# Kernel optimization log

Hardware: AMD Instinct MI355X
Metric: run time of the kernel (lower is better)

The kernel has to match this reference:

```python
import jax, jax.numpy as jnp
import numpy as np

IN_H = IN_W = 128
OUT_H = OUT_W = 512
CHUNK = 65536  # = 256*256, same chunk size as the torch while-loop
EPS = 1e-6


def _conv3(x, w, b):
    y = jax.lax.conv_general_dilated(x, w, (1, 1), ((1, 1), (1, 1)),
                                     dimension_numbers=('NCHW', 'OIHW', 'NCHW'))
    return y + b[None, :, None, None]


def _centers(n):
    # torch.arange(-1,1,2/n)+1/n  ==  cell centers in (-1,1)
    return (jnp.arange(n, dtype=jnp.float32) + 0.5) * (2.0 / n) - 1.0


def setup_inputs() -> dict:
    key = jax.random.key(0)
    ks = iter(jax.random.split(key, 40))
    rnd = lambda shape, s: jax.random.normal(next(ks), shape, jnp.float32) * s
    inp = {
        'x': jax.random.uniform(next(ks), (1, 3, IN_H, IN_W), jnp.float32),
        'output_size': jnp.array([OUT_H, OUT_W], dtype=jnp.int32),
        # EDSR encoder params
        'head_w': rnd((64, 3, 3, 3), 0.05), 'head_b': rnd((64,), 0.01),
        'rb_w': rnd((16, 2, 64, 64, 3, 3), 0.02), 'rb_b': rnd((16, 2, 64), 0.01),
        'tail_w': rnd((64, 64, 3, 3), 0.02), 'tail_b': rnd((64,), 0.01),
        # MLP 580 -> 256 -> 256 -> 256 -> 256 -> 3
        'mw0': rnd((580, 256), 0.04), 'mb0': rnd((256,), 0.01),
        'mw1': rnd((256, 256), 0.06), 'mb1': rnd((256,), 0.01),
        'mw2': rnd((256, 256), 0.06), 'mb2': rnd((256,), 0.01),
        'mw3': rnd((256, 256), 0.06), 'mb3': rnd((256,), 0.01),
        'mw4': rnd((256, 3), 0.06), 'mb4': rnd((3,), 0.01),
    }
    return inp


def reference(x, output_size, head_w, head_b, rb_w, rb_b, tail_w, tail_b,
              mw0, mb0, mw1, mb1, mw2, mb2, mw3, mb3, mw4, mb4):
    # ---- EDSR encoder (head conv + 16 resblocks + tail conv, residual) ----
    h0 = _conv3(x, head_w, head_b)

    def block(h, wb):
        w0, b0, w1, b1 = wb
        return h + _conv3(jax.nn.relu(_conv3(h, w0, b0)), w1, b1), None

    hb, _ = jax.lax.scan(block, h0, (rb_w[:, 0], rb_b[:, 0], rb_w[:, 1], rb_b[:, 1]))
    feat64 = h0 + _conv3(hb, tail_w, tail_b)  # [1,64,H,W]
    B, C, H, W = feat64.shape

    # im2col 3x3 pad 1 -> channel order (c, kh, kw), matching torch im2col.view
    p = jnp.pad(feat64, ((0, 0), (0, 0), (1, 1), (1, 1)))
    feat = jnp.stack([p[:, :, i:i + H, j:j + W]
                      for i in range(3) for j in range(3)],
                     axis=2).reshape(B, C * 9, H, W)  # [1,576,H,W]

    # normalized cell-center coordinate map of the feature grid: [2,H,W], (h,w)
    fg = jnp.stack(jnp.meshgrid(_centers(H), _centers(W), indexing='ij'))

    ws = (mw0, mw1, mw2, mw3, mw4)
    bs = (mb0, mb1, mb2, mb3, mb4)

    def mlp(t):
        for w, b in zip(ws[:-1], bs[:-1]):
            t = jax.nn.relu(t @ w + b)
        return t @ ws[-1] + bs[-1]

    dh, dw = 1.0 / H, 1.0 / W
    hw = jnp.array([H, W], jnp.float32)
    q_cell = jnp.array([2.0 * H / OUT_H, 2.0 * W / OUT_W], jnp.float32)
    fimg = feat[0]  # [576,H,W]

    def sample(img, gh, gw):
        # torch grid_sampler nearest, align_corners=False, round-half-to-even
        iy = jnp.clip(jnp.round(((gh + 1.0) * H - 1.0) * 0.5), 0, H - 1).astype(jnp.int32)
        ix = jnp.clip(jnp.round(((gw + 1.0) * W - 1.0) * 0.5), 0, W - 1).astype(jnp.int32)
        return img[:, iy, ix].T  # [P, C]

    def query_chunk(s_grid):  # [P,2] = (h,w) normalized coords
        preds, areas = [], []
        for r in (0, 1):
            for c in (0, 1):
                gh = jnp.clip(s_grid[:, 0] + (2.0 * r - 1.0) * dh, -1 + EPS, 1 - EPS)
                gw = jnp.clip(s_grid[:, 1] + (2.0 * c - 1.0) * dw, -1 + EPS, 1 - EPS)
                q_feat = sample(fimg, gh, gw)            # [P,576]
                q_grid = sample(fg, gh, gw)              # [P,2]
                rel = (s_grid - q_grid) * hw             # [P,2]
                inp = jnp.concatenate(
                    [q_feat, rel, jnp.broadcast_to(q_cell, rel.shape)], axis=-1)
                preds.append(mlp(inp))                   # [P,3]
                areas.append(jnp.abs(rel[:, 0] * rel[:, 1]))
        tot = areas[0] + areas[1] + areas[2] + areas[3] + 1e-9
        # LIIF local ensembling with swapped (diagonal) areas
        num = (preds[0] * areas[3][:, None] + preds[1] * areas[2][:, None]
               + preds[2] * areas[1][:, None] + preds[3] * areas[0][:, None])
        return num / tot[:, None]

    grid = jnp.stack(jnp.meshgrid(_centers(OUT_H), _centers(OUT_W), indexing='ij'),
                     axis=-1).reshape(-1, 2)             # [n,2]
    chunks = grid.reshape(-1, CHUNK, 2)                  # [nc,CHUNK,2]
    ys = jax.lax.map(query_chunk, chunks)                # [nc,CHUNK,3]
    y = ys.reshape(OUT_H, OUT_W, 3).transpose(2, 0, 1)[None]  # [1,3,OH,OW]
    return jnp.clip(y, 0.0, 1.0)
```

## Files before the change

kernel.cpp:

```cpp
#include <hip/hip_runtime.h>
#include <hip/hip_fp16.h>

typedef __attribute__((ext_vector_type(8))) _Float16 half8;
typedef __attribute__((ext_vector_type(4))) _Float16 half4;
typedef __attribute__((ext_vector_type(4))) float float4v;

#define NPIX 16384

__device__ inline half8 h8zero() {
    half8 z = {(_Float16)0, (_Float16)0, (_Float16)0, (_Float16)0,
               (_Float16)0, (_Float16)0, (_Float16)0, (_Float16)0};
    return z;
}

__global__ void pack_all(const float* __restrict__ rb_w, const float* __restrict__ tail_w,
                         const float* __restrict__ mw0, const float* __restrict__ mw1,
                         const float* __restrict__ mw2, const float* __restrict__ mw3,
                         const float* __restrict__ mw4, const float* __restrict__ mb0,
                         const float* __restrict__ x, const float* __restrict__ head_w,
                         const float* __restrict__ head_b,
                         _Float16* __restrict__ pwc, _Float16* __restrict__ pw0,
                         _Float16* __restrict__ pwm, float* __restrict__ b0p,
                         _Float16* __restrict__ h0) {
    int idx = blockIdx.x * 256 + threadIdx.x;
    if (idx < 1216512) {
        int ci = idx / 36864;
        int e  = idx % 36864;
        int j = e & 7, ln = (e >> 3) & 63, kcnt = e >> 9;
        int kc = kcnt % 18, ntc = kcnt / 18;
        int k = kc * 32 + (ln >> 4) * 8 + j;
        int nn = ntc * 16 + (ln & 15);
        int ij = k >> 6, c = k & 63;
        const float* src = (ci < 32) ? (rb_w + ci * 36864) : tail_w;
        pwc[idx] = (_Float16)src[(nn * 64 + c) * 9 + ij];
        return;
    }
    idx -= 1216512;
    if (idx < 147456) {
        int j = idx & 7, ln = (idx >> 3) & 63, kcnt = idx >> 9;
        int kc = kcnt % 18, ntc = kcnt / 18;
        int k = kc * 32 + (ln >> 4) * 8 + j;
        int nn = ntc * 16 + (ln & 15);
        int ij = k >> 6, c = k & 63;
        pw0[idx] = (_Float16)mw0[(c * 9 + ij) * 256 + nn];
        return;
    }
    idx -= 147456;
    if (idx < 200704) {
        if (idx < 196608) {
            int l = idx / 65536;
            int e = idx % 65536;
            int j = e & 7, ln = (e >> 3) & 63, kcnt = e >> 9;
            int kc = kcnt & 7, ntc = kcnt >> 3;
            int k = kc * 32 + (ln >> 4) * 8 + j;
            int nn = ntc * 16 + (ln & 15);
            const float* w = (l == 0) ? mw1 : ((l == 1) ? mw2 : mw3);
            pwm[idx] = (_Float16)w[k * 256 + nn];
        } else {
            int e = idx - 196608;
            int j = e & 7, ln = (e >> 3) & 63, kc = e >> 9;
            int k = kc * 32 + (ln >> 4) * 8 + j;
            int nn = ln & 15;
            pwm[idx] = (nn < 3) ? (_Float16)mw4[k * 3 + nn] : (_Float16)0.0f;
        }
        return;
    }
    idx -= 200704;
    if (idx < 256) {
        b0p[idx] = mb0[idx] + 0.5f * (mw0[578 * 256 + idx] + mw0[579 * 256 + idx]);
        return;
    }
    idx -= 256;
    if (idx < NPIX * 64) {
        int o = idx & 63, p = idx >> 6;
        int py = p >> 7, px = p & 127;
        float acc = head_b[o];
        #pragma unroll
        for (int c = 0; c < 3; ++c)
            #pragma unroll
            for (int i = 0; i < 3; ++i)
                #pragma unroll
                for (int jj = 0; jj < 3; ++jj) {
                    int y = py + i - 1, xx = px + jj - 1;
                    if (y >= 0 && y < 128 && xx >= 0 && xx < 128)
                        acc += x[c * 16384 + y * 128 + xx]
                             * head_w[((o * 3 + c) * 3 + i) * 3 + jj];
                }
        h0[idx] = (_Float16)acc;
    }
}

#define LDS_STRIDE 72

template <int DH, int DW, int SW, int SOFF, int RES, int ROFF, int INW>
__device__ __forceinline__ void conv_stage(
    const _Float16* __restrict__ src, _Float16* __restrict__ dst,
    _Float16* __restrict__ INb, const _Float16* __restrict__ resg,
    const _Float16* __restrict__ pw, const float* __restrict__ bias,
    int q, int r, int nb, int gy0, int gx0, _Float16* __restrict__ gout)
{
    half8 B[18];
    #pragma unroll
    for (int kc = 0; kc < 18; ++kc)
        B[kc] = *(const half8*)(pw + ((((nb >> 4) * 18 + kc) * 64 + (q << 4) + r) << 3));
    float bv = bias[nb + r];
    constexpr int NPXc = DH * DW;
    constexpr int NT = (NPXc + 15) >> 4;
    #pragma unroll 1
    for (int tl = 0; tl < NT; ++tl) {
        int pa = tl * 16 + r;
        int ca = pa < NPXc ? pa : NPXc - 1;
        int my = ca / DW, mx = ca % DW;
        float4v acc = {0.f, 0.f, 0.f, 0.f};
        #pragma unroll
        for (int kc = 0; kc < 18; ++kc) {
            int ij = kc >> 1;
            int di = ij / 3 - 1;
            int dj = ij % 3 - 1;
            int cb = ((kc & 1) << 5) + (q << 3);
            int sp = (my + 1 + di + SOFF) * SW + (mx + 1 + dj + SOFF);
            half8 a = *(const half8*)(src + sp * LDS_STRIDE + cb);
            acc = __builtin_amdgcn_mfma_f32_16x16x32_f16(a, B[kc], acc, 0, 0, 0);
        }
        #pragma unroll
        for (int reg = 0; reg < 4; ++reg) {
            int pc = tl * 16 + (q << 2) + reg;
            if (pc >= NPXc) continue;
            int dy = pc / DW, dx = pc % DW;
            int gy = gy0 + dy, gx = gx0 + dx;
            bool valid = (gy >= 0 && gy < 128 && gx >= 0 && gx < 128);
            if (RES == 0) {
                float v = fmaxf(acc[reg] + bv, 0.f);
                dst[pc * LDS_STRIDE + nb + r] = valid ? (_Float16)v : (_Float16)0.0f;
            } else if (RES == 1) {
                int sl = ((dy + ROFF) * INW + dx + ROFF) * LDS_STRIDE + nb + r;
                float v = acc[reg] + bv + (float)INb[sl];
                INb[sl] = valid ? (_Float16)v : (_Float16)0.0f;
            } else if (RES == 2) {
                int sl = ((dy + ROFF) * INW + dx + ROFF) * LDS_STRIDE + nb + r;
                float v = acc[reg] + bv + (float)INb[sl];
                gout[(((gy << 7) + gx) << 6) + nb + r] = (_Float16)v;
            } else {
                float v = acc[reg] + bv + (float)resg[(((gy << 7) + gx) << 6) + nb + r];
                gout[(((gy << 7) + gx) << 6) + nb + r] = (_Float16)v;
            }
        }
    }
}

__global__ __launch_bounds__(256, 3)
void rb_pair(const _Float16* __restrict__ img, const _Float16* __restrict__ pw,
             const float* __restrict__ bias, _Float16* __restrict__ out) {
    __shared__ _Float16 IN[192 * LDS_STRIDE];
    __shared__ _Float16 MID[140 * LDS_STRIDE];
    int t = threadIdx.x;
    int wave = t >> 6, lane = t & 63, q = lane >> 4, r = lane & 15;
    int tr = blockIdx.x >> 4, tc = blockIdx.x & 15;
    int ty0 = tr << 2, tx0 = tc << 3;
    int nb = wave << 4;

    #pragma unroll
    for (int i = 0; i < 6; ++i) {
        int idx = t + i * 256;
        int px = idx >> 3, c = idx & 7;
        int iy = px >> 4, ix = px & 15;
        int gy = ty0 - 4 + iy, gx = tx0 - 4 + ix;
        half8 v = h8zero();
        if (gy >= 0 && gy < 128 && gx >= 0 && gx < 128)
            v = *(const half8*)(img + (((gy << 7) + gx) << 6) + (c << 3));
        *(half8*)(IN + px * LDS_STRIDE + (c << 3)) = v;
    }
    __syncthreads();

    conv_stage<10, 14, 16, 0, 0, 0, 16>(IN, MID, IN, nullptr, pw, bias, q, r, nb,
                                        ty0 - 3, tx0 - 3, nullptr);
    __syncthreads();
    conv_stage<8, 12, 14, 0, 1, 2, 16>(MID, nullptr, IN, nullptr, pw + 36864, bias + 64,
                                       q, r, nb, ty0 - 2, tx0 - 2, nullptr);
    __syncthreads();
    conv_stage<6, 10, 16, 2, 0, 0, 16>(IN, MID, IN, nullptr, pw + 2 * 36864, bias + 128,
                                       q, r, nb, ty0 - 1, tx0 - 1, nullptr);
    __syncthreads();
    conv_stage<4, 8, 10, 0, 2, 4, 16>(MID, nullptr, IN, nullptr, pw + 3 * 36864, bias + 192,
                                      q, r, nb, ty0, tx0, out);
}

__global__ __launch_bounds__(256, 2)
void rb_tail(const _Float16* __restrict__ img, const _Float16* __restrict__ h0res,
             const _Float16* __restrict__ pw, const float* __restrict__ bias,
             const float* __restrict__ tail_b, _Float16* __restrict__ out) {
    __shared__ _Float16 IN[252 * LDS_STRIDE];
    __shared__ _Float16 MID[192 * LDS_STRIDE];
    int t = threadIdx.x;
    int wave = t >> 6, lane = t & 63, q = lane >> 4, r = lane & 15;
    int tr = blockIdx.x >> 4, tc = blockIdx.x & 15;
    int ty0 = tr << 2, tx0 = tc << 3;
    int nb = wave << 4;

    #pragma unroll
    for (int i = 0; i < 8; ++i) {
        int idx = t + i * 256;
        if (idx < 2016) {
            int px = idx >> 3, c = idx & 7;
            int iy = px / 18, ix = px % 18;
            int gy = ty0 - 5 + iy, gx = tx0 - 5 + ix;
            half8 v = h8zero();
            if (gy >= 0 && gy < 128 && gx >= 0 && gx < 128)
                v = *(const half8*)(img + (((gy << 7) + gx) << 6) + (c << 3));
            *(half8*)(IN + px * LDS_STRIDE + (c << 3)) = v;
        }
    }
    __syncthreads();

    conv_stage<12, 16, 18, 0, 0, 0, 18>(IN, MID, IN, nullptr, pw, bias, q, r, nb,
                                        ty0 - 4, tx0 - 4, nullptr);
    __syncthreads();
    conv_stage<10, 14, 16, 0, 1, 2, 18>(MID, nullptr, IN, nullptr, pw + 36864, bias + 64,
                                        q, r, nb, ty0 - 3, tx0 - 3, nullptr);
    __syncthreads();
    conv_stage<8, 12, 18, 2, 0, 0, 18>(IN, MID, IN, nullptr, pw + 2 * 36864, bias + 128,
                                       q, r, nb, ty0 - 2, tx0 - 2, nullptr);
    __syncthreads();
    conv_stage<6, 10, 12, 0, 1, 4, 18>(MID, nullptr, IN, nullptr, pw + 3 * 36864, bias + 192,
                                       q, r, nb, ty0 - 1, tx0 - 1, nullptr);
    __syncthreads();
    conv_stage<4, 8, 18, 4, 3, 0, 18>(IN, nullptr, IN, h0res, pw + 4 * 36864, tail_b,
                                      q, r, nb, ty0, tx0, out);
}

template <int NTOT, int MTPER, bool RELU, bool RES, bool F32OUT>
__global__ __launch_bounds__(256, 2)
void conv_mfma_r(const _Float16* __restrict__ img, const _Float16* __restrict__ pw,
                 const float* __restrict__ bias, const _Float16* res,
                 _Float16* outh, float* outf) {
    int wave = threadIdx.x >> 6, lane = threadIdx.x & 63;
    int q = lane >> 4, r = lane & 15;
    int nt, mt0;
    if constexpr (NTOT == 4) {
        nt = wave;
        mt0 = blockIdx.x * MTPER;
    } else {
        nt = (blockIdx.x & 3) * 4 + wave;
        mt0 = (blockIdx.x >> 2) * MTPER;
    }
    half8 B[18];
    #pragma unroll
    for (int kc = 0; kc < 18; ++kc)
        B[kc] = *(const half8*)(pw + (((nt * 18 + kc) * 64 + lane) << 3));
    int n = nt * 16 + r;
    float bv = bias[n];
    #pragma unroll
    for (int mi = 0; mi < MTPER; ++mi) {
        int mt = mt0 + mi;
        int p0 = mt * 16;
        int py = p0 >> 7;
        int pxl = (p0 & 127) + r;
        float4v acc = {0.f, 0.f, 0.f, 0.f};
        #pragma unroll
        for (int kc = 0; kc < 18; ++kc) {
            int ij = kc >> 1;
            int di = ij / 3 - 1;
            int dj = ij % 3 - 1;
            int cb = ((kc & 1) << 5) + (q << 3);
            int yy = py + di, xx = pxl + dj;
            half8 a = h8zero();
            if (yy >= 0 && yy < 128 && xx >= 0 && xx < 128)
                a = *(const half8*)(img + (((yy << 7) + xx) << 6) + cb);
            acc = __builtin_amdgcn_mfma_f32_16x16x32_f16(a, B[kc], acc, 0, 0, 0);
        }
        #pragma unroll
        for (int reg = 0; reg < 4; ++reg) {
            int p = p0 + (q << 2) + reg;
            float v = acc[reg] + bv;
            if (RES) v += (float)res[p * (NTOT * 16) + n];
            if (RELU) v = fmaxf(v, 0.f);
            if (F32OUT) outf[p * (NTOT * 16) + n] = v;
            else        outh[p * (NTOT * 16) + n] = (_Float16)v;
        }
    }
}

__global__ __launch_bounds__(512, 4)
void mlp_kernel(const float* __restrict__ apre, const float* __restrict__ mw0,
                const float* __restrict__ mb1, const float* __restrict__ mb2,
                const float* __restrict__ mb3, const float* __restrict__ mb4,
                const _Float16* __restrict__ pwm, const _Float16* __restrict__ pw4,
                float* __restrict__ out) {
    __shared__ _Float16 act[32768];
    __shared__ float sArea[128], sRelH[128], sRelW[128];
    __shared__ int sCell[128];
    __shared__ float sWh[256], sWw[256];

    int t = threadIdx.x;
    int bid = blockIdx.x;
    int logical = (bid & 7) * 1024 + (bid >> 3);
    int p0 = logical << 5;

    if (t < 128) {
        int lp = t >> 2, rc = t & 3;
        int p = p0 + lp;
        int oh = p >> 9, ow = p & 511;
        float sh = (oh + 0.5f) * (2.0f / 512.0f) - 1.0f;
        float sw = (ow + 0.5f) * (2.0f / 512.0f) - 1.0f;
        float gh = sh + (((rc >> 1) != 0) ? (1.0f / 128.0f) : (-1.0f / 128.0f));
        float gw = sw + (((rc & 1) != 0) ? (1.0f / 128.0f) : (-1.0f / 128.0f));
        const float lim = 1.0f - 1e-6f;
        gh = fminf(fmaxf(gh, -lim), lim);
        gw = fminf(fmaxf(gw, -lim), lim);
        int iy = (int)rintf(((gh + 1.0f) * 128.0f - 1.0f) * 0.5f);
        int ix = (int)rintf(((gw + 1.0f) * 128.0f - 1.0f) * 0.5f);
        iy = iy < 0 ? 0 : (iy > 127 ? 127 : iy);
        ix = ix < 0 ? 0 : (ix > 127 ? 127 : ix);
        float cy = (iy + 0.5f) * (2.0f / 128.0f) - 1.0f;
        float cx = (ix + 0.5f) * (2.0f / 128.0f) - 1.0f;
        float rh = (sh - cy) * 128.0f;
        float rw = (sw - cx) * 128.0f;
        sCell[t] = (iy << 7) + ix;
        sRelH[t] = rh; sRelW[t] = rw;
        sArea[t] = fabsf(rh * rw);
    }
    if (t < 256) {
        sWh[t] = mw0[576 * 256 + t];
        sWw[t] = mw0[577 * 256 + t];
    }
    __syncthreads();

    int wave = t >> 6, lane = t & 63, q = lane >> 4, r = lane & 15;

    {
        int s = (wave << 4) + r;
        float rh = sRelH[s], rw = sRelW[s];
        const float* ap = apre + ((size_t)sCell[s] << 8) + (q << 3);
        #pragma unroll
        for (int j = 0; j < 8; ++j) {
            int f0 = (j << 5) + (q << 3);
            float4v lo = *(const float4v*)(ap + (j << 5));
            float4v hi = *(const float4v*)(ap + (j << 5) + 4);
            half8 hv;
            #pragma unroll
            for (int kk = 0; kk < 4; ++kk) {
                float v = lo[kk] + rh * sWh[f0 + kk] + rw * sWw[f0 + kk];
                hv[kk] = (_Float16)fmaxf(v, 0.0f);
            }
            #pragma unroll
            for (int kk = 0; kk < 4; ++kk) {
                float v = hi[kk] + rh * sWh[f0 + 4 + kk] + rw * sWw[f0 + 4 + kk];
                hv[4 + kk] = (_Float16)fmaxf(v, 0.0f);
            }
            *(half8*)(act + ((((wave << 3) + j) * 64 + lane) << 3)) = hv;
        }
    }
    __syncthreads();

    float4v acc[2][8];
    #pragma unroll 1
    for (int l = 0; l < 3; ++l) {
        #pragma unroll
        for (int mti = 0; mti < 2; ++mti)
            #pragma unroll
            for (int nts = 0; nts < 8; ++nts)
                acc[mti][nts] = (float4v){0.f, 0.f, 0.f, 0.f};
        const _Float16* pw = pwm + l * 65536;
        for (int kc = 0; kc < 8; ++kc) {
            half8 A0 = *(const half8*)(pw + ((((wave * 2 + 0) * 8 + kc) * 64 + lane) << 3));
            half8 A1 = *(const half8*)(pw + ((((wave * 2 + 1) * 8 + kc) * 64 + lane) << 3));
            half8 Bf[4];
            #pragma unroll
            for (int nts = 0; nts < 4; ++nts)
                Bf[nts] = *(const half8*)(act + ((((nts << 3) + kc) * 64 + lane) << 3));
            #pragma unroll
            for (int nts = 0; nts < 4; ++nts) {
                acc[0][nts] = __builtin_amdgcn_mfma_f32_16x16x32_f16(A0, Bf[nts], acc[0][nts], 0, 0, 0);
                acc[1][nts] = __builtin_amdgcn_mfma_f32_16x16x32_f16(A1, Bf[nts], acc[1][nts], 0, 0, 0);
            }
            #pragma unroll
            for (int nts = 0; nts < 4; ++nts)
                Bf[nts] = *(const half8*)(act + (((((nts + 4) << 3) + kc) * 64 + lane) << 3));
            #pragma unroll
            for (int nts = 0; nts < 4; ++nts) {
                acc[0][nts + 4] = __builtin_amdgcn_mfma_f32_16x16x32_f16(A0, Bf[nts], acc[0][nts + 4], 0, 0, 0);
                acc[1][nts + 4] = __builtin_amdgcn_mfma_f32_16x16x32_f16(A1, Bf[nts], acc[1][nts + 4], 0, 0, 0);
            }
        }
        const float* mb = (l == 0) ? mb1 : ((l == 1) ? mb2 : mb3);
        __syncthreads();
        #pragma unroll
        for (int mti = 0; mti < 2; ++mti) {
            float4v bvv = *(const float4v*)(mb + (wave << 5) + mti * 16 + (q << 2));
            #pragma unroll
            for (int nts = 0; nts < 8; ++nts) {
                int base = ((((nts << 3) + wave) * 64
                             + ((mti * 2 + (q >> 1)) << 4) + r) << 3) + ((q & 1) << 2);
                half4 hv;
                #pragma unroll
                for (int reg = 0; reg < 4; ++reg)
                    hv[reg] = (_Float16)fmaxf(acc[mti][nts][reg] + bvv[reg], 0.0f);
                *(half4*)(act + base) = hv;
            }
        }
        __syncthreads();
    }

    {
        float4v af = {0.f, 0.f, 0.f, 0.f};
        #pragma unroll
        for (int kc = 0; kc < 8; ++kc) {
            half8 A = *(const half8*)(pw4 + ((kc * 64 + lane) << 3));
            half8 Bf = *(const half8*)(act + ((((wave << 3) + kc) * 64 + lane) << 3));
            af = __builtin_amdgcn_mfma_f32_16x16x32_f16(A, Bf, af, 0, 0, 0);
        }
        int s = (wave << 4) + r;
        int lp = s >> 2, rc = s & 3;
        float ar = sArea[(lp << 2) + (3 - rc)];
        float c0 = (af[0] + mb4[0]) * ar;
        float c1 = (af[1] + mb4[1]) * ar;
        float c2 = (af[2] + mb4[2]) * ar;
        c0 += __shfl_xor(c0, 1); c1 += __shfl_xor(c1, 1); c2 += __shfl_xor(c2, 1);
        float at = ar + __shfl_xor(ar, 1);
        c0 += __shfl_xor(c0, 2); c1 += __shfl_xor(c1, 2); c2 += __shfl_xor(c2, 2);
        at += __shfl_xor(at, 2);
        if (q == 0 && rc == 0) {
            float inv = 1.0f / (at + 1e-9f);
            out[p0 + lp]          = fminf(fmaxf(c0 * inv, 0.0f), 1.0f);
            out[262144 + p0 + lp] = fminf(fmaxf(c1 * inv, 0.0f), 1.0f);
            out[524288 + p0 + lp] = fminf(fmaxf(c2 * inv, 0.0f), 1.0f);
        }
    }
}

extern "C" void kernel_launch(void* const* d_in, const int* in_sizes, int n_in,
                              void* d_out, int out_size, void* d_ws, size_t ws_size,
                              hipStream_t stream) {
    (void)in_sizes; (void)n_in; (void)out_size; (void)ws_size;
    const float* x      = (const float*)d_in[0];
    const float* head_w = (const float*)d_in[2];
    const float* head_b = (const float*)d_in[3];
    const float* rb_w   = (const float*)d_in[4];
    const float* rb_b   = (const float*)d_in[5];
    const float* tail_w = (const float*)d_in[6];
    const float* tail_b = (const float*)d_in[7];
    const float* mw0    = (const float*)d_in[8];
    const float* mb0    = (const float*)d_in[9];
    const float* mw1    = (const float*)d_in[10];
    const float* mb1    = (const float*)d_in[11];
    const float* mw2    = (const float*)d_in[12];
    const float* mb2    = (const float*)d_in[13];
    const float* mw3    = (const float*)d_in[14];
    const float* mb3    = (const float*)d_in[15];
    const float* mw4    = (const float*)d_in[16];
    const float* mb4    = (const float*)d_in[17];
    float* out = (float*)d_out;

    char* w = (char*)d_ws;
    auto take = [&](size_t n) { char* p = w; w += (n + 255) & ~(size_t)255; return p; };
    _Float16* pwc  = (_Float16*)take(33u * 36864u * 2u);
    _Float16* pw0  = (_Float16*)take(147456u * 2u);
    _Float16* pwm  = (_Float16*)take(200704u * 2u);
    float*    b0p  = (float*)take(256u * 4u);
    _Float16* h0   = (_Float16*)take((size_t)NPIX * 64u * 2u);
    _Float16* hbuf = (_Float16*)take((size_t)NPIX * 64u * 2u);
    _Float16* tbuf = (_Float16*)take((size_t)NPIX * 64u * 2u);
    _Float16* feat = (_Float16*)take((size_t)NPIX * 64u * 2u);
    float*    apre = (float*)take((size_t)NPIX * 256u * 4u);

    pack_all<<<10209, 256, 0, stream>>>(rb_w, tail_w, mw0, mw1, mw2, mw3, mw4, mb0,
                                        x, head_w, head_b, pwc, pw0, pwm, b0p, h0);

    const _Float16* cur = h0;
    for (int p = 0; p < 7; ++p) {
        _Float16* dst = (p & 1) ? tbuf : hbuf;
        rb_pair<<<512, 256, 0, stream>>>(cur, pwc + 4 * p * 36864, rb_b + p * 256, dst);
        cur = dst;
    }
    rb_tail<<<512, 256, 0, stream>>>(cur, h0, pwc + 28 * 36864, rb_b + 7 * 256,
                                     tail_b, feat);
    conv_mfma_r<16, 4, false, false, true><<<1024, 256, 0, stream>>>(
        feat, pw0, b0p, nullptr, nullptr, apre);

    mlp_kernel<<<8192, 512, 0, stream>>>(apre, mw0, mb1, mb2, mb3, mb4,
                                         pwm, pwm + 196608, out);
}
```

Baseline: 758.7 us.

## Switch MLP hidden layers to 32x32x16 MFMA with repacked weights and activations

Repacks the MLP hidden-layer and output weights and the LDS activation layout so each wave computes a 32-row output slice with 32x32x16 MFMA instructions instead of pairs of 16x16x32 MFMAs. This halves the number of LDS B-fragment loads per MFMA FLOP and issues fewer, larger matrix instructions. The final 256->3 layer now runs on only 4 of the 8 waves with a 32-wide tile that wastes more of the padded columns. Pack sizes and the launch grid are adjusted to match the new layout.

```diff
diff --git a/kernel.cpp b/kernel.cpp
--- a/kernel.cpp
+++ b/kernel.cpp
@@ -4,6 +4,7 @@
 typedef __attribute__((ext_vector_type(8))) _Float16 half8;
 typedef __attribute__((ext_vector_type(4))) _Float16 half4;
 typedef __attribute__((ext_vector_type(4))) float float4v;
+typedef __attribute__((ext_vector_type(16))) float float16v;
 
 #define NPIX 16384
 
@@ -46,26 +47,26 @@
         return;
     }
     idx -= 147456;
-    if (idx < 200704) {
+    if (idx < 204800) {
         if (idx < 196608) {
             int l = idx / 65536;
             int e = idx % 65536;
-            int j = e & 7, ln = (e >> 3) & 63, kcnt = e >> 9;
-            int kc = kcnt & 7, ntc = kcnt >> 3;
-            int k = kc * 32 + (ln >> 4) * 8 + j;
-            int nn = ntc * 16 + (ln & 15);
+            int j = e & 7, ln = (e >> 3) & 63, rest = e >> 9;
+            int kc = rest & 15, wv = rest >> 4;
+            int k = kc * 16 + ((ln >> 5) << 3) + j;
+            int nn = (wv << 5) + (ln & 31);
             const float* w = (l == 0) ? mw1 : ((l == 1) ? mw2 : mw3);
             pwm[idx] = (_Float16)w[k * 256 + nn];
         } else {
             int e = idx - 196608;
             int j = e & 7, ln = (e >> 3) & 63, kc = e >> 9;
-            int k = kc * 32 + (ln >> 4) * 8 + j;
-            int nn = ln & 15;
+            int k = kc * 16 + ((ln >> 5) << 3) + j;
+            int nn = ln & 31;
             pwm[idx] = (nn < 3) ? (_Float16)mw4[k * 3 + nn] : (_Float16)0.0f;
         }
         return;
     }
-    idx -= 200704;
+    idx -= 204800;
     if (idx < 256) {
         b0p[idx] = mb0[idx] + 0.5f * (mw0[578 * 256 + idx] + mw0[579 * 256 + idx]);
         return;
@@ -325,17 +326,20 @@
     }
     __syncthreads();
 
-    int wave = t >> 6, lane = t & 63, q = lane >> 4, r = lane & 15;
+    int wave = t >> 6, lane = t & 63;
+    int col = lane & 31, h = lane >> 5;
 
     {
-        int s = (wave << 4) + r;
+        int sgrp = wave & 3, fhalf = wave >> 2;
+        int s = (sgrp << 5) + col;
         float rh = sRelH[s], rw = sRelW[s];
-        const float* ap = apre + ((size_t)sCell[s] << 8) + (q << 3);
-        #pragma unroll
-        for (int j = 0; j < 8; ++j) {
-            int f0 = (j << 5) + (q << 3);
-            float4v lo = *(const float4v*)(ap + (j << 5));
-            float4v hi = *(const float4v*)(ap + (j << 5) + 4);
+        int fbase = fhalf << 7;
+        const float* ap = apre + ((size_t)sCell[s] << 8) + fbase + (h << 3);
+        #pragma unroll
+        for (int c = 0; c < 8; ++c) {
+            int f0 = fbase + (c << 4) + (h << 3);
+            float4v lo = *(const float4v*)(ap + (c << 4));
+            float4v hi = *(const float4v*)(ap + (c << 4) + 4);
             half8 hv;
             #pragma unroll
             for (int kk = 0; kk < 4; ++kk) {
@@ -347,69 +351,59 @@
                 float v = hi[kk] + rh * sWh[f0 + 4 + kk] + rw * sWw[f0 + 4 + kk];
                 hv[4 + kk] = (_Float16)fmaxf(v, 0.0f);
             }
-            *(half8*)(act + ((((wave << 3) + j) * 64 + lane) << 3)) = hv;
-        }
-    }
-    __syncthreads();
-
-    float4v acc[2][8];
+            int X = (sgrp << 4) + (fhalf << 3) + c;
+            *(half8*)(act + ((X * 64 + lane) << 3)) = hv;
+        }
+    }
+    __syncthreads();
+
+    float16v acc[4];
     #pragma unroll 1
     for (int l = 0; l < 3; ++l) {
         #pragma unroll
-        for (int mti = 0; mti < 2; ++mti)
-            #pragma unroll
-            for (int nts = 0; nts < 8; ++nts)
-                acc[mti][nts] = (float4v){0.f, 0.f, 0.f, 0.f};
+        for (int nts = 0; nts < 4; ++nts)
+            #pragma unroll
+            for (int e = 0; e < 16; ++e)
+                acc[nts][e] = 0.0f;
         const _Float16* pw = pwm + l * 65536;
-        for (int kc = 0; kc < 8; ++kc) {
-            half8 A0 = *(const half8*)(pw + ((((wave * 2 + 0) * 8 + kc) * 64 + lane) << 3));
-            half8 A1 = *(const half8*)(pw + ((((wave * 2 + 1) * 8 + kc) * 64 + lane) << 3));
-            half8 Bf[4];
-            #pragma unroll
-            for (int nts = 0; nts < 4; ++nts)
-                Bf[nts] = *(const half8*)(act + ((((nts << 3) + kc) * 64 + lane) << 3));
+        for (int kc = 0; kc < 16; ++kc) {
+            half8 A = *(const half8*)(pw + ((((wave << 4) + kc) * 64 + lane) << 3));
             #pragma unroll
             for (int nts = 0; nts < 4; ++nts) {
-                acc[0][nts] = __builtin_amdgcn_mfma_f32_16x16x32_f16(A0, Bf[nts], acc[0][nts], 0, 0, 0);
-                acc[1][nts] = __builtin_amdgcn_mfma_f32_16x16x32_f16(A1, Bf[nts], acc[1][nts], 0, 0, 0);
-            }
-            #pragma unroll
-            for (int nts = 0; nts < 4; ++nts)
-                Bf[nts] = *(const half8*)(act + (((((nts + 4) << 3) + kc) * 64 + lane) << 3));
-            #pragma unroll
-            for (int nts = 0; nts < 4; ++nts) {
-                acc[0][nts + 4] = __builtin_amdgcn_mfma_f32_16x16x32_f16(A0, Bf[nts], acc[0][nts + 4], 0, 0, 0);
-                acc[1][nts + 4] = __builtin_amdgcn_mfma_f32_16x16x32_f16(A1, Bf[nts], acc[1][nts + 4], 0, 0, 0);
+                half8 Bf = *(const half8*)(act + ((((nts << 4) + kc) * 64 + lane) << 3));
+                acc[nts] = __builtin_amdgcn_mfma_f32_32x32x16_f16(A, Bf, acc[nts], 0, 0, 0);
             }
         }
         const float* mb = (l == 0) ? mb1 : ((l == 1) ? mb2 : mb3);
         __syncthreads();
         #pragma unroll
-        for (int mti = 0; mti < 2; ++mti) {
-            float4v bvv = *(const float4v*)(mb + (wave << 5) + mti * 16 + (q << 2));
-            #pragma unroll
-            for (int nts = 0; nts < 8; ++nts) {
-                int base = ((((nts << 3) + wave) * 64
-                             + ((mti * 2 + (q >> 1)) << 4) + r) << 3) + ((q & 1) << 2);
+        for (int g = 0; g < 4; ++g) {
+            float4v bvv = *(const float4v*)(mb + (wave << 5) + (g << 3) + (h << 2));
+            #pragma unroll
+            for (int nts = 0; nts < 4; ++nts) {
+                int X = (nts << 4) + (wave << 1) + (g >> 1);
+                int lp2 = col + ((g & 1) << 5);
                 half4 hv;
                 #pragma unroll
-                for (int reg = 0; reg < 4; ++reg)
-                    hv[reg] = (_Float16)fmaxf(acc[mti][nts][reg] + bvv[reg], 0.0f);
-                *(half4*)(act + base) = hv;
+                for (int rr = 0; rr < 4; ++rr)
+                    hv[rr] = (_Float16)fmaxf(acc[nts][g * 4 + rr] + bvv[rr], 0.0f);
+                *(half4*)(act + (((X * 64 + lp2) << 3) + (h << 2))) = hv;
             }
         }
         __syncthreads();
     }
 
-    {
-        float4v af = {0.f, 0.f, 0.f, 0.f};
-        #pragma unroll
-        for (int kc = 0; kc < 8; ++kc) {
+    if (wave < 4) {
+        float16v af;
+        #pragma unroll
+        for (int e = 0; e < 16; ++e) af[e] = 0.0f;
+        #pragma unroll 1
+        for (int kc = 0; kc < 16; ++kc) {
             half8 A = *(const half8*)(pw4 + ((kc * 64 + lane) << 3));
-            half8 Bf = *(const half8*)(act + ((((wave << 3) + kc) * 64 + lane) << 3));
-            af = __builtin_amdgcn_mfma_f32_16x16x32_f16(A, Bf, af, 0, 0, 0);
-        }
-        int s = (wave << 4) + r;
+            half8 Bf = *(const half8*)(act + ((((wave << 4) + kc) * 64 + lane) << 3));
+            af = __builtin_amdgcn_mfma_f32_32x32x16_f16(A, Bf, af, 0, 0, 0);
+        }
+        int s = (wave << 5) + col;
         int lp = s >> 2, rc = s & 3;
         float ar = sArea[(lp << 2) + (3 - rc)];
         float c0 = (af[0] + mb4[0]) * ar;
@@ -419,7 +413,7 @@
         float at = ar + __shfl_xor(ar, 1);
         c0 += __shfl_xor(c0, 2); c1 += __shfl_xor(c1, 2); c2 += __shfl_xor(c2, 2);
         at += __shfl_xor(at, 2);
-        if (q == 0 && rc == 0) {
+        if (h == 0 && rc == 0) {
             float inv = 1.0f / (at + 1e-9f);
             out[p0 + lp]          = fminf(fmaxf(c0 * inv, 0.0f), 1.0f);
             out[262144 + p0 + lp] = fminf(fmaxf(c1 * inv, 0.0f), 1.0f);
@@ -455,7 +449,7 @@
     auto take = [&](size_t n) { char* p = w; w += (n + 255) & ~(size_t)255; return p; };
     _Float16* pwc  = (_Float16*)take(33u * 36864u * 2u);
     _Float16* pw0  = (_Float16*)take(147456u * 2u);
-    _Float16* pwm  = (_Float16*)take(200704u * 2u);
+    _Float16* pwm  = (_Float16*)take(204800u * 2u);
     float*    b0p  = (float*)take(256u * 4u);
     _Float16* h0   = (_Float16*)take((size_t)NPIX * 64u * 2u);
     _Float16* hbuf = (_Float16*)take((size_t)NPIX * 64u * 2u);
@@ -463,7 +457,7 @@
     _Float16* feat = (_Float16*)take((size_t)NPIX * 64u * 2u);
     float*    apre = (float*)take((size_t)NPIX * 256u * 4u);
 
-    pack_all<<<10209, 256, 0, stream>>>(rb_w, tail_w, mw0, mw1, mw2, mw3, mw4, mb0,
+    pack_all<<<10225, 256, 0, stream>>>(rb_w, tail_w, mw0, mw1, mw2, mw3, mw4, mb0,
                                         x, head_w, head_b, pwc, pw0, pwm, b0p, h0);
 
     const _Float16* cur = h0;
```

Result: slower. 798.2 us (+5.2%).
